# Kernel optimization log

Hardware: AMD Instinct MI355X
Metric: run time of the kernel (lower is better)

The kernel has to match this reference:

```python
import jax, jax.numpy as jnp
import numpy as np

N_NODES = 100000
N_EDGES = 3200000
D_IN, D_HID, D_OUT = 256, 256, 256
B, V, C = 64, 50, 64
DEC_H1, DEC_H2, N_CLS = 512, 256, 1000
NEG_INF = -1e9


def setup_inputs() -> dict:
    key = jax.random.key(0)
    ks = jax.random.split(key, 20)
    s = lambda d: 1.0 / np.sqrt(d)
    return {
        'edge_index': jax.random.randint(ks[0], (2, N_EDGES), 0, N_NODES, dtype=jnp.int64 if jax.config.jax_enable_x64 else jnp.int32),
        'edge_weight': jax.random.uniform(ks[1], (N_EDGES,), dtype=jnp.float32),
        'codes_x': jax.random.randint(ks[2], (B, V, C), 0, N_NODES, dtype=jnp.int64 if jax.config.jax_enable_x64 else jnp.int32),
        'node_emb': jax.random.normal(ks[3], (N_NODES, D_IN), jnp.float32) * 0.02,
        'W1': jax.random.normal(ks[4], (D_IN, D_HID), jnp.float32) * s(D_IN),
        'b1': jnp.zeros((D_HID,), jnp.float32),
        'W2': jax.random.normal(ks[5], (D_HID, D_OUT), jnp.float32) * s(D_HID),
        'b2': jnp.zeros((D_OUT,), jnp.float32),
        'Wv': jax.random.normal(ks[6], (D_OUT, D_OUT), jnp.float32) * s(D_OUT),
        'uv': jax.random.normal(ks[7], (D_OUT,), jnp.float32) * s(D_OUT),
        'Wp': jax.random.normal(ks[8], (D_OUT, D_OUT), jnp.float32) * s(D_OUT),
        'up': jax.random.normal(ks[9], (D_OUT,), jnp.float32) * s(D_OUT),
        'Wd1': jax.random.normal(ks[10], (D_OUT, DEC_H1), jnp.float32) * s(D_OUT),
        'bd1': jnp.zeros((DEC_H1,), jnp.float32),
        'Wd2': jax.random.normal(ks[11], (DEC_H1, DEC_H2), jnp.float32) * s(DEC_H1),
        'bd2': jnp.zeros((DEC_H2,), jnp.float32),
        'Wd3': jax.random.normal(ks[12], (DEC_H2, N_CLS), jnp.float32) * s(DEC_H2),
        'bd3': jnp.zeros((N_CLS,), jnp.float32),
    }


def reference(edge_index, edge_weight, codes_x, node_emb, W1, b1, W2, b2,
              Wv, uv, Wp, up, Wd1, bd1, Wd2, bd2, Wd3, bd3):
    n = node_emb.shape[0]
    src, dst = edge_index[0], edge_index[1]

    def agg(x):  # weighted message passing: out_i = sum_{e: dst=i} w_e * x[src_e]
        return jax.ops.segment_sum(x[src] * edge_weight[:, None], dst, num_segments=n)

    # 2-layer weighted GCN over the code ontology graph (dropout in eval mode)
    h = jax.nn.relu(agg(node_emb) @ W1 + b1)          # [N, D_hid]
    emb = agg(h) @ W2 + b2                             # [N, D_out]

    # Ragged per-visit code attention, vectorized with masks (code id 0 = padding)
    code_mask = codes_x > 0                            # [B, V, C]
    ce = emb[codes_x]                                  # [B, V, C, D]
    ev = jnp.tanh(jnp.einsum('bvcd,de->bvce', ce, Wv)) @ uv   # [B, V, C]
    av = jax.nn.softmax(jnp.where(code_mask, ev, NEG_INF), axis=-1)
    vemb = jnp.einsum('bvc,bvcd->bvd', av, ce)         # [B, V, D]
    visit_mask = code_mask.any(-1)                     # [B, V]
    vemb = jnp.where(visit_mask[..., None], vemb, 0.0)

    # Per-patient visit attention over valid visits only
    ep = jnp.tanh(vemb @ Wp) @ up                      # [B, V]
    ap = jax.nn.softmax(jnp.where(visit_mask, ep, NEG_INF), axis=-1)
    pemb = jnp.einsum('bv,bvd->bd', ap, vemb)          # [B, D]
    pemb = jnp.where(visit_mask.any(-1)[:, None], pemb, 0.0)  # empty patient -> zeros

    # Decoder MLP classifier (train_type='direct')
    h1 = jax.nn.relu(pemb @ Wd1 + bd1)
    h2 = jax.nn.relu(h1 @ Wd2 + bd2)
    return h2 @ Wd3 + bd3                              # [B, n_classes]
```

## Files before the change

### kernel.cpp

```cpp
#include <hip/hip_runtime.h>
#include <hip/hip_bf16.h>
#include <math.h>


#define D 256
#define BPAT 64
#define VIS 50
#define CODES 64
#define NEG_INF -1e9f
#define MPAD 100096
#define BINB 32
#define NBIN 3125

typedef unsigned short ushort_t;
typedef short short8 __attribute__((ext_vector_type(8)));
typedef float f32x4 __attribute__((ext_vector_type(4)));

__device__ __forceinline__ float blo(unsigned u) { return __uint_as_float(u << 16); }
__device__ __forceinline__ float bhi(unsigned u) { return __uint_as_float(u & 0xffff0000u); }
__device__ __forceinline__ float bf2f(ushort_t u) { return __uint_as_float((unsigned)u << 16); }
__device__ __forceinline__ ushort_t f2bfu(float f) {
    __hip_bfloat16 h = __float2bfloat16(f);
    return *reinterpret_cast<ushort_t*>(&h);
}
__device__ __forceinline__ unsigned pack2(float a, float b) {
    return (unsigned)f2bfu(a) | ((unsigned)f2bfu(b) << 16);
}


__global__ __launch_bounds__(512) void bin_count_kernel(
    const int* __restrict__ ei, int* __restrict__ bincount, int ne) {
    __shared__ int h[NBIN];
    for (int i = threadIdx.x; i < NBIN; i += 512) h[i] = 0;
    __syncthreads();
    int stride = gridDim.x * 512;
    for (int e = blockIdx.x * 512 + threadIdx.x; e < ne; e += stride)
        atomicAdd(&h[ei[(size_t)ne + e] >> 5], 1);
    __syncthreads();
    for (int i = threadIdx.x; i < NBIN; i += 512) {
        int c = h[i];
        if (c) atomicAdd(&bincount[i], c);
    }
}

__global__ __launch_bounds__(64) void bin_scan_kernel(
    const int* __restrict__ bincount, int* __restrict__ binstart,
    int* __restrict__ bincursor, int* __restrict__ rp, int ne, int nn) {
    __shared__ int carry;
    int lane = threadIdx.x;
    if (lane == 0) carry = 0;
    __syncthreads();
    for (int base = 0; base < NBIN; base += 64) {
        int i = base + lane;
        int v = (i < NBIN) ? bincount[i] : 0;
        int x = v;
        #pragma unroll
        for (int d = 1; d < 64; d <<= 1) {
            int y = __shfl_up(x, (unsigned)d, 64);
            if (lane >= d) x += y;
        }
        int c = carry;
        if (i < NBIN) { int ex = c + x - v; binstart[i] = ex; bincursor[i] = ex; }
        __syncthreads();
        if (lane == 63) carry = c + x;
        __syncthreads();
    }
    if (lane == 0) { binstart[NBIN] = ne; rp[nn] = ne; }
}

__global__ __launch_bounds__(512) void partition_kernel(
    const int* __restrict__ ei, const float* __restrict__ ew,
    int* __restrict__ bincursor, uint2* __restrict__ ptmp, int ne) {
    __shared__ int h[NBIN];
    __shared__ int base_[NBIN];
    for (int i = threadIdx.x; i < NBIN; i += 512) h[i] = 0;
    __syncthreads();
    int stride = gridDim.x * 512;
    for (int e = blockIdx.x * 512 + threadIdx.x; e < ne; e += stride)
        atomicAdd(&h[ei[(size_t)ne + e] >> 5], 1);
    __syncthreads();
    for (int i = threadIdx.x; i < NBIN; i += 512) {
        int c = h[i];
        base_[i] = c ? atomicAdd(&bincursor[i], c) : 0;
        h[i] = 0;
    }
    __syncthreads();
    for (int e = blockIdx.x * 512 + threadIdx.x; e < ne; e += stride) {
        int dd = ei[(size_t)ne + e];
        int ss = ei[e];
        float w = ew[e];
        int bin = dd >> 5;
        int r = atomicAdd(&h[bin], 1);
        ptmp[base_[bin] + r] =
            make_uint2((unsigned)ss | ((unsigned)(dd & 31) << 17),
                       __float_as_uint(w));
    }
}

__global__ __launch_bounds__(256) void binsort_kernel(
    const uint2* __restrict__ ptmp, const int* __restrict__ binstart,
    uint2* __restrict__ epair, int* __restrict__ rp) {
    int b = blockIdx.x;
    int tid = threadIdx.x;
    int beg = binstart[b], end = binstart[b + 1];
    __shared__ int cnt[BINB];
    __shared__ int cur[BINB];
    if (tid < BINB) cnt[tid] = 0;
    __syncthreads();
    for (int i = beg + tid; i < end; i += 256)
        atomicAdd(&cnt[(ptmp[i].x >> 17) & 31], 1);
    __syncthreads();
    if (tid < BINB) {
        int v = cnt[tid];
        int x = v;
        #pragma unroll
        for (int d = 1; d < BINB; d <<= 1) {
            int y = __shfl_up(x, (unsigned)d, BINB);
            if (tid >= d) x += y;
        }
        int start = beg + x - v;
        cur[tid] = start;
        rp[b * BINB + tid] = start;
    }
    __syncthreads();
    for (int i = beg + tid; i < end; i += 256) {
        uint2 p = ptmp[i];
        int dl = (p.x >> 17) & 31;
        int pos = atomicAdd(&cur[dl], 1);
        epair[pos] = make_uint2(p.x & 0x1FFFF, p.y);
    }
}

__global__ void cvt_node_kernel(const float* __restrict__ in, ushort_t* __restrict__ out,
                                long n_valid, long n_total) {
    long g = (long)blockIdx.x * blockDim.x + threadIdx.x;
    long ng = n_total >> 2;
    for (long i = g; i < ng; i += (long)gridDim.x * blockDim.x) {
        long e = i << 2;
        uint2 o;
        if (e < n_valid) {
            float4 v = ((const float4*)in)[i];
            o.x = pack2(v.x, v.y);
            o.y = pack2(v.z, v.w);
        } else {
            o.x = 0u; o.y = 0u;
        }
        ((uint2*)out)[i] = o;
    }
}

__global__ __launch_bounds__(256) void transpose_w_kernel(
    const float* __restrict__ W, ushort_t* __restrict__ Wt) {
    __shared__ float t[32][33];
    int bx = blockIdx.x * 32;
    int by = blockIdx.y * 32;
    int lx = threadIdx.x & 31, ly = threadIdx.x >> 5;
    #pragma unroll
    for (int i = 0; i < 32; i += 8)
        t[ly + i][lx] = W[(size_t)(by + ly + i) * 256 + bx + lx];
    __syncthreads();
    #pragma unroll
    for (int i = 0; i < 32; i += 8)
        Wt[(size_t)(bx + ly + i) * 256 + by + lx] = f2bfu(t[lx][ly + i]);
}

__device__ __forceinline__ void acc8(float* a, uint4 v, float w) {
    a[0] += w * blo(v.x); a[1] += w * bhi(v.x);
    a[2] += w * blo(v.y); a[3] += w * bhi(v.y);
    a[4] += w * blo(v.z); a[5] += w * bhi(v.z);
    a[6] += w * blo(v.w); a[7] += w * bhi(v.w);
}

__global__ __launch_bounds__(256) void agg_bf16_kernel(
    const ushort_t* __restrict__ x, const int* __restrict__ rp,
    const uint2* __restrict__ ep, ushort_t* __restrict__ out, int n) {
    int wv = (int)(((size_t)blockIdx.x * blockDim.x + threadIdx.x) >> 6);
    int lane = threadIdx.x & 63;
    if (wv >= n) return;
    int half = lane >> 5;
    int l32 = lane & 31;
    int beg = rp[wv], end = rp[wv + 1];
    float a[8] = {};
    int e = beg;
    for (; e + 8 <= end; e += 8) {
        uint2 p0 = ep[e + half];
        uint2 p1 = ep[e + 2 + half];
        uint2 p2 = ep[e + 4 + half];
        uint2 p3 = ep[e + 6 + half];
        uint4 v0 = ((const uint4*)(x + (size_t)p0.x * D))[l32];
        uint4 v1 = ((const uint4*)(x + (size_t)p1.x * D))[l32];
        uint4 v2 = ((const uint4*)(x + (size_t)p2.x * D))[l32];
        uint4 v3 = ((const uint4*)(x + (size_t)p3.x * D))[l32];
        acc8(a, v0, __uint_as_float(p0.y));
        acc8(a, v1, __uint_as_float(p1.y));
        acc8(a, v2, __uint_as_float(p2.y));
        acc8(a, v3, __uint_as_float(p3.y));
    }
    for (; e + 2 <= end; e += 2) {
        uint2 p0 = ep[e + half];
        uint4 v0 = ((const uint4*)(x + (size_t)p0.x * D))[l32];
        acc8(a, v0, __uint_as_float(p0.y));
    }
    if (e < end) {
        uint2 p0 = ep[e];
        uint4 v0 = ((const uint4*)(x + (size_t)p0.x * D))[l32];
        acc8(a, v0, half ? 0.f : __uint_as_float(p0.y));
    }
    #pragma unroll
    for (int j = 0; j < 8; ++j) a[j] += __shfl_xor(a[j], 32, 64);
    if (half == 0) {
        uint4 o;
        o.x = pack2(a[0], a[1]); o.y = pack2(a[2], a[3]);
        o.z = pack2(a[4], a[5]); o.w = pack2(a[6], a[7]);
        ((uint4*)(out + (size_t)wv * D))[l32] = o;
    }
}

template<int MODE>
__global__ __launch_bounds__(512) void mfma_gemm_kernel(
    const ushort_t* __restrict__ A, const ushort_t* __restrict__ Wt,
    const float* __restrict__ bias, ushort_t* __restrict__ out,
    const float* __restrict__ u, float* __restrict__ tout, int mvalid) {
    __shared__ __align__(16) ushort_t As[128 * 32];
    __shared__ __align__(16) ushort_t Bs[256 * 32];
    __shared__ float s_t[128];
    const int tid = threadIdx.x;
    const int lane = tid & 63;
    const int wv = tid >> 6;
    const int wr = wv >> 2, wc = wv & 3;
    const size_t brow = (size_t)blockIdx.x * 128;

    const int ra = tid >> 2, ca = tid & 3;
    const int rb1 = ra + 128;
    const int csa = ca ^ ((ra >> 1) & 3);
    const ushort_t* gA  = A  + (brow + ra) * 256 + ca * 8;
    const ushort_t* gB0 = Wt + (size_t)ra  * 256 + ca * 8;
    const ushort_t* gB1 = Wt + (size_t)rb1 * 256 + ca * 8;
    ushort_t* lA  = As + ra * 32 + csa * 8;
    ushort_t* lB0 = Bs + ra * 32 + csa * 8;
    ushort_t* lB1 = Bs + rb1 * 32 + csa * 8;

    const int g = lane >> 4, rl = lane & 15;
    int aoff[4], boff[4];
    #pragma unroll
    for (int m = 0; m < 4; ++m) {
        int row = wr * 64 + m * 16 + rl;
        aoff[m] = row * 32 + (g ^ ((row >> 1) & 3)) * 8;
    }
    #pragma unroll
    for (int n = 0; n < 4; ++n) {
        int row = wc * 64 + n * 16 + rl;
        boff[n] = row * 32 + (g ^ ((row >> 1) & 3)) * 8;
    }

    if (MODE == 2 && tid < 128) s_t[tid] = 0.f;

    f32x4 acc[4][4] = {};
    uint4 va  = *(const uint4*)gA;
    uint4 vb0 = *(const uint4*)gB0;
    uint4 vb1 = *(const uint4*)gB1;

    for (int ks = 0; ks < 8; ++ks) {
        *(uint4*)lA = va; *(uint4*)lB0 = vb0; *(uint4*)lB1 = vb1;
        __syncthreads();
        if (ks < 7) {
            int k0 = (ks + 1) * 32;
            va  = *(const uint4*)(gA + k0);
            vb0 = *(const uint4*)(gB0 + k0);
            vb1 = *(const uint4*)(gB1 + k0);
        }
        short8 af[4], bfv[4];
        #pragma unroll
        for (int m = 0; m < 4; ++m) af[m] = *(const short8*)(As + aoff[m]);
        #pragma unroll
        for (int n = 0; n < 4; ++n) bfv[n] = *(const short8*)(Bs + boff[n]);
        #pragma unroll
        for (int m = 0; m < 4; ++m)
            #pragma unroll
            for (int n = 0; n < 4; ++n)
                acc[m][n] = __builtin_amdgcn_mfma_f32_16x16x32_bf16(
                    af[m], bfv[n], acc[m][n], 0, 0, 0);
        __syncthreads();
    }

    if (MODE == 2) {
        float uvv[4];
        #pragma unroll
        for (int n = 0; n < 4; ++n) uvv[n] = u[wc * 64 + n * 16 + rl];
        #pragma unroll
        for (int m = 0; m < 4; ++m) {
            #pragma unroll
            for (int r = 0; r < 4; ++r) {
                float v = 0.f;
                #pragma unroll
                for (int n = 0; n < 4; ++n) v += tanhf(acc[m][n][r]) * uvv[n];
                v += __shfl_xor(v, 1, 64);
                v += __shfl_xor(v, 2, 64);
                v += __shfl_xor(v, 4, 64);
                v += __shfl_xor(v, 8, 64);
                if (rl == 0) atomicAdd(&s_t[wr * 64 + m * 16 + g * 4 + r], v);
            }
        }
        __syncthreads();
        if (tid < 128 && brow + tid < (size_t)mvalid) tout[brow + tid] = s_t[tid];
    } else {
        #pragma unroll
        for (int m = 0; m < 4; ++m) {
            #pragma unroll
            for (int r = 0; r < 4; ++r) {
                size_t row = brow + wr * 64 + m * 16 + g * 4 + r;
                #pragma unroll
                for (int n = 0; n < 4; ++n) {
                    int col = wc * 64 + n * 16 + rl;
                    float v = acc[m][n][r] + bias[col];
                    if (MODE == 0) v = fmaxf(v, 0.f);
                    out[row * 256 + col] = f2bfu(v);
                }
            }
        }
    }
}

__global__ __launch_bounds__(256) void code_attn_kernel(
    const int* __restrict__ codes, const float* __restrict__ t,
    const ushort_t* __restrict__ emb, ushort_t* __restrict__ vembB,
    int* __restrict__ vmask) {
    int bv = blockIdx.x;
    int tid = threadIdx.x;
    __shared__ int s_codes[CODES];
    __shared__ float s_av[CODES];
    __shared__ int s_valid;
    if (tid < 64) {
        int c = codes[(size_t)bv * CODES + tid];
        s_codes[tid] = c;
        float e = (c > 0) ? t[c] : NEG_INF;
        float m = e;
        #pragma unroll
        for (int d = 32; d; d >>= 1) m = fmaxf(m, __shfl_xor(m, d, 64));
        float ex = expf(e - m);
        float s = ex;
        #pragma unroll
        for (int d = 32; d; d >>= 1) s += __shfl_xor(s, d, 64);
        s_av[tid] = ex / s;
        if (tid == 0) s_valid = (m > -1e8f) ? 1 : 0;
    }
    __syncthreads();
    float acc = 0.f;
    #pragma unroll 4
    for (int c = 0; c < CODES; ++c) {
        int node = s_codes[c];
        if (node > 0) acc += s_av[c] * bf2f(emb[(size_t)node * D + tid]);
    }
    int valid = s_valid;
    vembB[(size_t)bv * D + tid] = f2bfu(valid ? acc : 0.f);
    if (tid == 0) vmask[bv] = valid;
}

__global__ __launch_bounds__(256) void patient_kernel(
    const ushort_t* __restrict__ vembB, const float* __restrict__ epr,
    const int* __restrict__ vmask, float* __restrict__ pemb) {
    int b = blockIdx.x;
    int tid = threadIdx.x;
    __shared__ float s_ap[VIS];
    __shared__ int s_any;
    if (tid < 64) {
        float e = -3e38f;
        if (tid < VIS) e = vmask[b * VIS + tid] ? epr[b * VIS + tid] : NEG_INF;
        float m = e;
        #pragma unroll
        for (int d = 32; d; d >>= 1) m = fmaxf(m, __shfl_xor(m, d, 64));
        float ex = (tid < VIS) ? expf(e - m) : 0.f;
        float s = ex;
        #pragma unroll
        for (int d = 32; d; d >>= 1) s += __shfl_xor(s, d, 64);
        if (tid < VIS) s_ap[tid] = ex / s;
        if (tid == 0) s_any = (m > -1e8f) ? 1 : 0;
    }
    __syncthreads();
    float acc = 0.f;
    for (int v = 0; v < VIS; ++v)
        acc += s_ap[v] * bf2f(vembB[((size_t)b * VIS + v) * D + tid]);
    pemb[b * D + tid] = s_any ? acc : 0.f;
}

__global__ __launch_bounds__(256) void gemm_rowcol(
    const float* __restrict__ A, const float* __restrict__ W,
    const float* __restrict__ bias, float* __restrict__ C,
    int M, int N, int K, int act) {
    int row = blockIdx.x;
    int col = blockIdx.y * 256 + threadIdx.x;
    if (col >= N) return;
    const float* a = A + (size_t)row * K;
    float acc = bias ? bias[col] : 0.f;
    #pragma unroll 4
    for (int k = 0; k < K; ++k) acc = fmaf(a[k], W[(size_t)k * N + col], acc);
    if (act == 1) acc = fmaxf(acc, 0.f);
    C[(size_t)row * N + col] = acc;
}

extern "C" void kernel_launch(void* const* d_in, const int* in_sizes, int n_in,
                              void* d_out, int out_size, void* d_ws, size_t ws_size,
                              hipStream_t stream) {
    const int* edge_index    = (const int*)d_in[0];
    const float* edge_weight = (const float*)d_in[1];
    const int* codes         = (const int*)d_in[2];
    const float* node_emb    = (const float*)d_in[3];
    const float* W1 = (const float*)d_in[4];
    const float* b1 = (const float*)d_in[5];
    const float* W2 = (const float*)d_in[6];
    const float* b2 = (const float*)d_in[7];
    const float* Wv = (const float*)d_in[8];
    const float* uv = (const float*)d_in[9];
    const float* Wp = (const float*)d_in[10];
    const float* up = (const float*)d_in[11];
    const float* Wd1 = (const float*)d_in[12];
    const float* bd1 = (const float*)d_in[13];
    const float* Wd2 = (const float*)d_in[14];
    const float* bd2 = (const float*)d_in[15];
    const float* Wd3 = (const float*)d_in[16];
    const float* bd3 = (const float*)d_in[17];

    const int NE = in_sizes[1];
    const int NN = in_sizes[3] / D;

    char* ws = (char*)d_ws;
    size_t off = 0;
    auto alloc = [&](size_t bytes) -> void* {
        void* p = ws + off;
        off += (bytes + 255) & ~(size_t)255;
        return p;
    };
    ushort_t* nbf  = (ushort_t*)alloc((size_t)MPAD * D * 2);
    ushort_t* aggb = (ushort_t*)alloc((size_t)MPAD * D * 2);
    ushort_t* embB = (ushort_t*)alloc((size_t)MPAD * D * 2);
    uint2* ptmp   = (uint2*)alloc((size_t)NE * 8);
    uint2* epair  = (uint2*)alloc((size_t)NE * 8);
    int* bincount = (int*)alloc((size_t)NBIN * 4);
    int* binstart = (int*)alloc((size_t)(NBIN + 1) * 4);
    int* bincursor= (int*)alloc((size_t)NBIN * 4);
    int* rp       = (int*)alloc((size_t)(NN + 1) * 4);
    ushort_t* W1t = (ushort_t*)alloc(256 * 256 * 2);
    ushort_t* W2t = (ushort_t*)alloc(256 * 256 * 2);
    ushort_t* Wvt = (ushort_t*)alloc(256 * 256 * 2);
    ushort_t* Wpt = (ushort_t*)alloc(256 * 256 * 2);
    float* tbuf  = (float*)alloc((size_t)NN * 4);
    ushort_t* vembB = (ushort_t*)alloc((size_t)BPAT * VIS * D * 2);
    int*   vmask = (int*)  alloc((size_t)BPAT * VIS * 4);
    float* epr   = (float*)alloc((size_t)BPAT * VIS * 4);
    float* pemb  = (float*)alloc((size_t)BPAT * D * 4);
    float* h1    = (float*)alloc((size_t)BPAT * 512 * 4);
    float* h2    = (float*)alloc((size_t)BPAT * D * 4);
    (void)ws_size; (void)n_in; (void)out_size;

    const int ab = NN / 4;

    hipMemsetAsync(bincount, 0, (size_t)NBIN * 4, stream);
    bin_count_kernel<<<256, 512, 0, stream>>>(edge_index, bincount, NE);
    bin_scan_kernel<<<1, 64, 0, stream>>>(bincount, binstart, bincursor, rp, NE, NN);
    partition_kernel<<<128, 512, 0, stream>>>(edge_index, edge_weight,
                                              bincursor, ptmp, NE);
    binsort_kernel<<<NBIN, 256, 0, stream>>>(ptmp, binstart, epair, rp);

    cvt_node_kernel<<<2048, 256, 0, stream>>>(node_emb, nbf, (long)NN * D, (long)MPAD * D);
    dim3 tg(8, 8);
    transpose_w_kernel<<<tg, 256, 0, stream>>>(W1, W1t);
    transpose_w_kernel<<<tg, 256, 0, stream>>>(W2, W2t);
    transpose_w_kernel<<<tg, 256, 0, stream>>>(Wv, Wvt);
    transpose_w_kernel<<<tg, 256, 0, stream>>>(Wp, Wpt);

    agg_bf16_kernel<<<ab, 256, 0, stream>>>(nbf, rp, epair, aggb, NN);
    mfma_gemm_kernel<0><<<MPAD / 128, 512, 0, stream>>>(
        aggb, W1t, b1, nbf, nullptr, nullptr, 0);

    agg_bf16_kernel<<<ab, 256, 0, stream>>>(nbf, rp, epair, aggb, NN);
    mfma_gemm_kernel<1><<<MPAD / 128, 512, 0, stream>>>(
        aggb, W2t, b2, embB, nullptr, nullptr, 0);

    mfma_gemm_kernel<2><<<MPAD / 128, 512, 0, stream>>>(
        embB, Wvt, nullptr, nullptr, uv, tbuf, NN);

    code_attn_kernel<<<BPAT * VIS, 256, 0, stream>>>(codes, tbuf, embB, vembB, vmask);

    mfma_gemm_kernel<2><<<BPAT * VIS / 128, 512, 0, stream>>>(
        vembB, Wpt, nullptr, nullptr, up, epr, BPAT * VIS);

    patient_kernel<<<BPAT, 256, 0, stream>>>(vembB, epr, vmask, pemb);
    gemm_rowcol<<<dim3(BPAT, 2), 256, 0, stream>>>(pemb, Wd1, bd1, h1, BPAT, 512, D, 1);
    gemm_rowcol<<<dim3(BPAT, 1), 256, 0, stream>>>(h1, Wd2, bd2, h2, BPAT, D, 512, 1);
    gemm_rowcol<<<dim3(BPAT, 4), 256, 0, stream>>>(h2, Wd3, bd3, (float*)d_out, BPAT, 1000, D, 0);
}
```

Before: 924.4 us.

## Stage binsort edges in LDS, merge weight transposes, deepen aggregation unroll

Binsort now loads each bin's edges once into shared memory (up to 1536 entries) instead of reading ptmp twice from global memory, and falls back to the old path for larger bins. The four weight-transpose launches become one launch using blockIdx.z to pick the matrix, which saves launch overhead. The aggregation gather loop is unrolled to 16 edges per iteration, with a 4-edge remainder loop, to keep more loads in flight. The risks are higher register pressure in the aggregation kernel and a 12KB LDS buffer in binsort that may reduce occupancy.

```diff
diff --git a/kernel.cpp b/kernel.cpp
--- a/kernel.cpp
+++ b/kernel.cpp
@@ -11,6 +11,7 @@
 #define MPAD 100096
 #define BINB 32
 #define NBIN 3125
+#define SORTCAP 1536
 
 typedef unsigned short ushort_t;
 typedef short short8 __attribute__((ext_vector_type(8)));
@@ -103,31 +104,61 @@
     int b = blockIdx.x;
     int tid = threadIdx.x;
     int beg = binstart[b], end = binstart[b + 1];
+    int nE = end - beg;
+    __shared__ uint2 sbuf[SORTCAP];
     __shared__ int cnt[BINB];
     __shared__ int cur[BINB];
     if (tid < BINB) cnt[tid] = 0;
     __syncthreads();
-    for (int i = beg + tid; i < end; i += 256)
-        atomicAdd(&cnt[(ptmp[i].x >> 17) & 31], 1);
-    __syncthreads();
-    if (tid < BINB) {
-        int v = cnt[tid];
-        int x = v;
-        #pragma unroll
-        for (int d = 1; d < BINB; d <<= 1) {
-            int y = __shfl_up(x, (unsigned)d, BINB);
-            if (tid >= d) x += y;
-        }
-        int start = beg + x - v;
-        cur[tid] = start;
-        rp[b * BINB + tid] = start;
-    }
-    __syncthreads();
-    for (int i = beg + tid; i < end; i += 256) {
-        uint2 p = ptmp[i];
-        int dl = (p.x >> 17) & 31;
-        int pos = atomicAdd(&cur[dl], 1);
-        epair[pos] = make_uint2(p.x & 0x1FFFF, p.y);
+    if (nE <= SORTCAP) {
+        for (int i = tid; i < nE; i += 256) {
+            uint2 p = ptmp[beg + i];
+            sbuf[i] = p;
+            atomicAdd(&cnt[(p.x >> 17) & 31], 1);
+        }
+        __syncthreads();
+        if (tid < BINB) {
+            int v = cnt[tid];
+            int x = v;
+            #pragma unroll
+            for (int d = 1; d < BINB; d <<= 1) {
+                int y = __shfl_up(x, (unsigned)d, BINB);
+                if (tid >= d) x += y;
+            }
+            int start = beg + x - v;
+            cur[tid] = start;
+            rp[b * BINB + tid] = start;
+        }
+        __syncthreads();
+        for (int i = tid; i < nE; i += 256) {
+            uint2 p = sbuf[i];
+            int dl = (p.x >> 17) & 31;
+            int pos = atomicAdd(&cur[dl], 1);
+            epair[pos] = make_uint2(p.x & 0x1FFFF, p.y);
+        }
+    } else {
+        for (int i = beg + tid; i < end; i += 256)
+            atomicAdd(&cnt[(ptmp[i].x >> 17) & 31], 1);
+        __syncthreads();
+        if (tid < BINB) {
+            int v = cnt[tid];
+            int x = v;
+            #pragma unroll
+            for (int d = 1; d < BINB; d <<= 1) {
+                int y = __shfl_up(x, (unsigned)d, BINB);
+                if (tid >= d) x += y;
+            }
+            int start = beg + x - v;
+            cur[tid] = start;
+            rp[b * BINB + tid] = start;
+        }
+        __syncthreads();
+        for (int i = beg + tid; i < end; i += 256) {
+            uint2 p = ptmp[i];
+            int dl = (p.x >> 17) & 31;
+            int pos = atomicAdd(&cur[dl], 1);
+            epair[pos] = make_uint2(p.x & 0x1FFFF, p.y);
+        }
     }
 }
 
@@ -149,8 +180,19 @@
     }
 }
 
-__global__ __launch_bounds__(256) void transpose_w_kernel(
-    const float* __restrict__ W, ushort_t* __restrict__ Wt) {
+__global__ __launch_bounds__(256) void transpose_w4_kernel(
+    const float* __restrict__ Wa, const float* __restrict__ Wb,
+    const float* __restrict__ Wc, const float* __restrict__ Wd,
+    ushort_t* __restrict__ Ta, ushort_t* __restrict__ Tb,
+    ushort_t* __restrict__ Tc, ushort_t* __restrict__ Td) {
+    const float* W;
+    ushort_t* Wt;
+    switch (blockIdx.z) {
+        case 0: W = Wa; Wt = Ta; break;
+        case 1: W = Wb; Wt = Tb; break;
+        case 2: W = Wc; Wt = Tc; break;
+        default: W = Wd; Wt = Td; break;
+    }
     __shared__ float t[32][33];
     int bx = blockIdx.x * 32;
     int by = blockIdx.y * 32;
@@ -182,19 +224,39 @@
     int beg = rp[wv], end = rp[wv + 1];
     float a[8] = {};
     int e = beg;
-    for (; e + 8 <= end; e += 8) {
+    for (; e + 16 <= end; e += 16) {
         uint2 p0 = ep[e + half];
         uint2 p1 = ep[e + 2 + half];
         uint2 p2 = ep[e + 4 + half];
         uint2 p3 = ep[e + 6 + half];
+        uint2 p4 = ep[e + 8 + half];
+        uint2 p5 = ep[e + 10 + half];
+        uint2 p6 = ep[e + 12 + half];
+        uint2 p7 = ep[e + 14 + half];
         uint4 v0 = ((const uint4*)(x + (size_t)p0.x * D))[l32];
         uint4 v1 = ((const uint4*)(x + (size_t)p1.x * D))[l32];
         uint4 v2 = ((const uint4*)(x + (size_t)p2.x * D))[l32];
         uint4 v3 = ((const uint4*)(x + (size_t)p3.x * D))[l32];
+        uint4 v4 = ((const uint4*)(x + (size_t)p4.x * D))[l32];
+        uint4 v5 = ((const uint4*)(x + (size_t)p5.x * D))[l32];
+        uint4 v6 = ((const uint4*)(x + (size_t)p6.x * D))[l32];
+        uint4 v7 = ((const uint4*)(x + (size_t)p7.x * D))[l32];
         acc8(a, v0, __uint_as_float(p0.y));
         acc8(a, v1, __uint_as_float(p1.y));
         acc8(a, v2, __uint_as_float(p2.y));
         acc8(a, v3, __uint_as_float(p3.y));
+        acc8(a, v4, __uint_as_float(p4.y));
+        acc8(a, v5, __uint_as_float(p5.y));
+        acc8(a, v6, __uint_as_float(p6.y));
+        acc8(a, v7, __uint_as_float(p7.y));
+    }
+    for (; e + 4 <= end; e += 4) {
+        uint2 p0 = ep[e + half];
+        uint2 p1 = ep[e + 2 + half];
+        uint4 v0 = ((const uint4*)(x + (size_t)p0.x * D))[l32];
+        uint4 v1 = ((const uint4*)(x + (size_t)p1.x * D))[l32];
+        acc8(a, v0, __uint_as_float(p0.y));
+        acc8(a, v1, __uint_as_float(p1.y));
     }
     for (; e + 2 <= end; e += 2) {
         uint2 p0 = ep[e + half];
@@ -462,11 +524,8 @@
     binsort_kernel<<<NBIN, 256, 0, stream>>>(ptmp, binstart, epair, rp);
 
     cvt_node_kernel<<<2048, 256, 0, stream>>>(node_emb, nbf, (long)NN * D, (long)MPAD * D);
-    dim3 tg(8, 8);
-    transpose_w_kernel<<<tg, 256, 0, stream>>>(W1, W1t);
-    transpose_w_kernel<<<tg, 256, 0, stream>>>(W2, W2t);
-    transpose_w_kernel<<<tg, 256, 0, stream>>>(Wv, Wvt);
-    transpose_w_kernel<<<tg, 256, 0, stream>>>(Wp, Wpt);
+    transpose_w4_kernel<<<dim3(8, 8, 4), 256, 0, stream>>>(
+        W1, W2, Wv, Wp, W1t, W2t, Wvt, Wpt);
 
     agg_bf16_kernel<<<ab, 256, 0, stream>>>(nbf, rp, epair, aggb, NN);
     mfma_gemm_kernel<0><<<MPAD / 128, 512, 0, stream>>>(
```

Result: no change. 911.1 us (-1.4%).
